# Optimization experiments

Measured on AMD Instinct MI355X. Metric: run time of the kernel, lower is better.

Reference implementation:

```python
import jax, jax.numpy as jnp
import numpy as np

N = 100000      # nodes
E = 1600000     # edges (avg degree 16)
D_IN, D_H, D_OUT = 128, 64, 40


def setup_inputs() -> dict:
    key = jax.random.key(0)
    ks = jax.random.split(key, 9)
    x = jax.random.normal(ks[0], (N, D_IN), dtype=jnp.float32)
    edge_index = jax.random.randint(ks[1], (2, E), 0, N)
    affected_mask = jax.random.randint(ks[2], (N,), 0, 2).astype(bool)
    # GCNConv weights stored as [in, out]
    Wc1 = jax.random.normal(ks[3], (D_IN, D_H), jnp.float32) / np.sqrt(D_IN)
    bc1 = jax.random.normal(ks[4], (D_H,), jnp.float32) * 0.01
    Wc2 = jax.random.normal(ks[5], (D_H, D_OUT), jnp.float32) / np.sqrt(D_H)
    bc2 = jax.random.normal(ks[6], (D_OUT,), jnp.float32) * 0.01
    # deletion operators initialized to identity (per nn.init.eye_/zeros_)
    Wd1 = jnp.eye(D_H, dtype=jnp.float32)
    bd1 = jnp.zeros((D_H,), jnp.float32)
    Wd2 = jnp.eye(D_OUT, dtype=jnp.float32)
    bd2 = jnp.zeros((D_OUT,), jnp.float32)
    return {"x": x, "edge_index": edge_index, "affected_mask": affected_mask,
            "Wc1": Wc1, "bc1": bc1, "Wc2": Wc2, "bc2": bc2,
            "Wd1": Wd1, "bd1": bd1, "Wd2": Wd2, "bd2": bd2}


def _gcn_norm(edge_index, n):
    # add self loops, compute symmetric normalization coefficients
    loop = jnp.arange(n)
    src = jnp.concatenate([edge_index[0], loop])
    dst = jnp.concatenate([edge_index[1], loop])
    deg = jax.ops.segment_sum(jnp.ones_like(src, jnp.float32), dst, num_segments=n)
    dinv = jnp.where(deg > 0, jax.lax.rsqrt(deg), 0.0)
    norm = dinv[src] * dinv[dst]  # [E+N]
    return src, dst, norm


def _gcn_conv(h, src, dst, norm, W, b, n):
    hw = h @ W                              # [N, d_out]
    msg = hw[src] * norm[:, None]           # gather + scale  [E+N, d_out]
    return jax.ops.segment_sum(msg, dst, num_segments=n) + b


def reference(x, edge_index, affected_mask, Wc1, bc1, Wc2, bc2, Wd1, bd1, Wd2, bd2):
    n = x.shape[0]
    src, dst, norm = _gcn_norm(edge_index, n)
    h = jax.nn.relu(_gcn_conv(x, src, dst, norm, Wc1, bc1, n))
    # eval-mode dropout == identity
    # deletion op 1: masked gather -> linear -> scatter == masked select
    m1 = affected_mask[:, None]
    h_del = jnp.where(m1, h @ Wd1.T + bd1, h)
    out = _gcn_conv(h_del, src, dst, norm, Wc2, bc2, n)
    out_del = jnp.where(m1, out @ Wd2.T + bd2, out)
    return out_del
```

## Files before the change

### kernel.cpp

```cpp
#include <hip/hip_runtime.h>

#define D_IN  128
#define D_H   64
#define D_OUT 40

__device__ __forceinline__ float bf_lo(unsigned u){ return __uint_as_float(u << 16); }
__device__ __forceinline__ float bf_hi(unsigned u){ return __uint_as_float(u & 0xFFFF0000u); }
__device__ __forceinline__ unsigned bf_pack(float a, float b){
  unsigned ua = __float_as_uint(a), ub = __float_as_uint(b);
  unsigned lo = (ua + 0x7FFFu + ((ua >> 16) & 1u)) >> 16;
  unsigned hi = (ub + 0x7FFFu + ((ub >> 16) & 1u)) & 0xFFFF0000u;
  return hi | lo;
}


__launch_bounds__(256)
static __global__ void k_degpos(const int* __restrict__ dst, int* __restrict__ deg,
                                int* __restrict__ pos, int E){
  int base = (blockIdx.x*256 + threadIdx.x) * 4;
  if (base + 4 <= E){
    int4 d = *(const int4*)(dst + base);
    int4 p;
    p.x = atomicAdd(&deg[d.x], 1);
    p.y = atomicAdd(&deg[d.y], 1);
    p.z = atomicAdd(&deg[d.z], 1);
    p.w = atomicAdd(&deg[d.w], 1);
    *(int4*)(pos + base) = p;
  } else {
    for (int i = base; i < E; i++) pos[i] = atomicAdd(&deg[dst[i]], 1);
  }
}

static __global__ void k_scan1(const int* __restrict__ deg, int* __restrict__ incl,
                               int* __restrict__ bsums, int n){
  __shared__ int s[1024];
  int t = threadIdx.x; int g = blockIdx.x*1024 + t;
  int v = (g < n) ? deg[g] : 0;
  s[t] = v; __syncthreads();
  for (int off = 1; off < 1024; off <<= 1){
    int u = (t >= off) ? s[t-off] : 0; __syncthreads();
    s[t] += u; __syncthreads();
  }
  if (g < n) incl[g] = s[t];
  if (t == 1023) bsums[blockIdx.x] = s[1023];
}

static __global__ void k_scan2(int* bsums, int nb){
  __shared__ int s[128];
  int t = threadIdx.x;
  int v = (t < nb) ? bsums[t] : 0;
  s[t] = v; __syncthreads();
  for (int off = 1; off < 128; off <<= 1){
    int u = (t >= off) ? s[t-off] : 0; __syncthreads();
    s[t] += u; __syncthreads();
  }
  if (t < nb) bsums[t] = s[t] - v;
}

static __global__ void k_scan3(const int* __restrict__ deg, int* __restrict__ rs,
                               const int* __restrict__ bsums,
                               float* __restrict__ dinv, int n){
  int t = threadIdx.x; int g = blockIdx.x*1024 + t;
  if (g < n){
    int excl = rs[g] - deg[g] + bsums[blockIdx.x];
    rs[g] = excl;
    dinv[g] = rsqrtf((float)(deg[g] + 1));
  }
}

__launch_bounds__(256)
static __global__ void k_scatter(const int* __restrict__ src, const int* __restrict__ dst,
                                 const int* __restrict__ pos, const int* __restrict__ rs,
                                 int* __restrict__ col, int E){
  int base = (blockIdx.x*256 + threadIdx.x) * 4;
  if (base + 4 <= E){
    int4 d = *(const int4*)(dst + base);
    int4 s = *(const int4*)(src + base);
    int4 p = *(const int4*)(pos + base);
    col[rs[d.x] + p.x] = s.x;
    col[rs[d.y] + p.y] = s.y;
    col[rs[d.z] + p.z] = s.z;
    col[rs[d.w] + p.w] = s.w;
  } else {
    for (int i = base; i < E; i++) col[rs[dst[i]] + pos[i]] = src[i];
  }
}


static __global__ void k_pre(const float* __restrict__ Wd1, const float* __restrict__ bd1,
                             const float* __restrict__ Wc2, float* __restrict__ M,
                             float* __restrict__ bvec){
  int t = threadIdx.x;
  for (int i = t; i < D_H*D_OUT; i += 256){
    int q = i / D_OUT, j = i % D_OUT;
    float s = 0.f;
    for (int k = 0; k < D_H; k++) s += Wd1[k*D_H + q] * Wc2[k*D_OUT + j];
    M[i] = s;
  }
  if (t < D_OUT){
    float s = 0.f;
    for (int k = 0; k < D_H; k++) s += bd1[k] * Wc2[k*D_OUT + t];
    bvec[t] = s;
  }
}


__launch_bounds__(256)
static __global__ void k_gemm1(const float* __restrict__ x, const float* __restrict__ Wc1,
                               const float* __restrict__ dinv,
                               unsigned short* __restrict__ hws1b, int n){
  __shared__ float Wl[D_IN*D_H];
  __shared__ float xs[32][D_IN+1];
  int t = threadIdx.x;
  int base = blockIdx.x*32;
  for (int i = t; i < D_IN*D_H; i += 256) Wl[i] = Wc1[i];
  for (int i = t; i < 32*D_IN; i += 256){
    int r = i >> 7, c = i & 127;
    int node = base + r;
    xs[r][c] = (node < n) ? x[(size_t)node*D_IN + c] : 0.f;
  }
  __syncthreads();
  int nl = t >> 3, j0 = (t & 7)*8;
  int node = base + nl;
  if (node >= n) return;
  float acc[8] = {0,0,0,0,0,0,0,0};
  #pragma unroll 4
  for (int k = 0; k < D_IN; k++){
    float xv = xs[nl][k];
    #pragma unroll
    for (int jj = 0; jj < 8; jj++) acc[jj] += xv * Wl[k*D_H + j0 + jj];
  }
  float dv = dinv[node];
  uint4 o;
  o.x = bf_pack(acc[0]*dv, acc[1]*dv);
  o.y = bf_pack(acc[2]*dv, acc[3]*dv);
  o.z = bf_pack(acc[4]*dv, acc[5]*dv);
  o.w = bf_pack(acc[6]*dv, acc[7]*dv);
  *(uint4*)(hws1b + (size_t)node*D_H + j0) = o;
}


__launch_bounds__(256)
static __global__ void k_agg1(const unsigned short* __restrict__ hws1b, const int* __restrict__ rs,
                              const int* __restrict__ deg, const int* __restrict__ col,
                              const float* __restrict__ dinv, const float* __restrict__ bc1,
                              float* __restrict__ h, int n){
  int t = threadIdx.x;
  int wave = t >> 6, lane = t & 63;
  int node = blockIdx.x*4 + wave;
  if (node >= n) return;
  int grp = lane >> 4, fl = lane & 15;
  const uint2* g2 = (const uint2*)hws1b;
  float a0=0.f, a1=0.f, a2=0.f, a3=0.f;
  if (grp == 0){
    uint2 v = g2[(size_t)node*16 + fl];
    a0 += bf_lo(v.x); a1 += bf_hi(v.x); a2 += bf_lo(v.y); a3 += bf_hi(v.y);
  }
  int s0 = rs[node], cnt = deg[node];
  #pragma unroll 4
  for (int e0 = 0; e0 < cnt; e0 += 4){
    int sl = e0 + grp;
    if (sl < cnt){
      int s = col[s0 + sl];
      uint2 v = g2[(size_t)s*16 + fl];
      a0 += bf_lo(v.x); a1 += bf_hi(v.x); a2 += bf_lo(v.y); a3 += bf_hi(v.y);
    }
  }
  a0 += __shfl_xor(a0, 16, 64); a1 += __shfl_xor(a1, 16, 64);
  a2 += __shfl_xor(a2, 16, 64); a3 += __shfl_xor(a3, 16, 64);
  a0 += __shfl_xor(a0, 32, 64); a1 += __shfl_xor(a1, 32, 64);
  a2 += __shfl_xor(a2, 32, 64); a3 += __shfl_xor(a3, 32, 64);
  if (grp == 0){
    float dv = dinv[node];
    float4 b = ((const float4*)bc1)[fl];
    float4 o;
    o.x = fmaxf(a0*dv + b.x, 0.f);
    o.y = fmaxf(a1*dv + b.y, 0.f);
    o.z = fmaxf(a2*dv + b.z, 0.f);
    o.w = fmaxf(a3*dv + b.w, 0.f);
    ((float4*)h)[(size_t)node*16 + fl] = o;
  }
}


__launch_bounds__(128)
static __global__ void k_gemm2(const float* __restrict__ h, const unsigned char* __restrict__ mask,
                               const float* __restrict__ Mmat, const float* __restrict__ bvec,
                               const float* __restrict__ Wc2, const float* __restrict__ dinv,
                               unsigned short* __restrict__ hws2b, int n){
  __shared__ float Ms[D_H*D_OUT];
  __shared__ float Ws[D_H*D_OUT];
  __shared__ float bv[D_OUT];
  __shared__ float hs[128*(D_H+1)];
  int t = threadIdx.x;
  int base = blockIdx.x*128;
  for (int i = t; i < D_H*D_OUT; i += 128){ Ms[i] = Mmat[i]; Ws[i] = Wc2[i]; }
  if (t < D_OUT) bv[t] = bvec[t];
  for (int i = t; i < 128*D_H; i += 128){
    int r = i >> 6, c = i & 63;
    int node = base + r;
    hs[r*(D_H+1) + c] = (node < n) ? h[(size_t)node*D_H + c] : 0.f;
  }
  __syncthreads();
  int node = base + t;
  if (node >= n) return;
  bool m = mask[node] != 0;
  const float* Wp = m ? Ms : Ws;
  float acc[D_OUT];
  #pragma unroll
  for (int j = 0; j < D_OUT; j++) acc[j] = m ? bv[j] : 0.f;
  const float* hrow = &hs[t*(D_H+1)];
  for (int q = 0; q < D_H; q++){
    float hv = hrow[q];
    #pragma unroll
    for (int j = 0; j < D_OUT; j++) acc[j] += hv * Wp[q*D_OUT + j];
  }
  float dv = dinv[node];
  unsigned short* op = hws2b + (size_t)node*D_OUT;
  #pragma unroll
  for (int k = 0; k < 5; k++){
    uint4 o;
    o.x = bf_pack(acc[k*8+0]*dv, acc[k*8+1]*dv);
    o.y = bf_pack(acc[k*8+2]*dv, acc[k*8+3]*dv);
    o.z = bf_pack(acc[k*8+4]*dv, acc[k*8+5]*dv);
    o.w = bf_pack(acc[k*8+6]*dv, acc[k*8+7]*dv);
    *(uint4*)(op + k*8) = o;
  }
}


__launch_bounds__(256)
static __global__ void k_agg2(const unsigned short* __restrict__ hws2b, const int* __restrict__ rs,
                              const int* __restrict__ deg, const int* __restrict__ col,
                              const float* __restrict__ dinv, const float* __restrict__ bc2,
                              const unsigned char* __restrict__ mask,
                              const float* __restrict__ Wd2, const float* __restrict__ bd2,
                              float* __restrict__ out, int n){
  __shared__ float4 wds4[D_OUT*11];
  __shared__ float  bds[D_OUT];
  __shared__ float4 os4[4][11];
  int t = threadIdx.x;
  for (int i = t; i < D_OUT*10; i += 256){
    int j = i / 10, q = i % 10;
    const float* wr = Wd2 + j*D_OUT + q*4;
    wds4[j*11 + q] = make_float4(wr[0], wr[1], wr[2], wr[3]);
  }
  if (t < D_OUT) bds[t] = bd2[t];
  __syncthreads();
  int wave = t >> 6, lane = t & 63;
  int node = blockIdx.x*4 + wave;
  if (node >= n) return;
  int grp = lane >> 4, fl = lane & 15;
  bool fa = fl < 10;
  const uint2* g2 = (const uint2*)hws2b;
  float a0=0.f, a1=0.f, a2=0.f, a3=0.f;
  if (grp == 0 && fa){
    uint2 v = g2[(size_t)node*10 + fl];
    a0 += bf_lo(v.x); a1 += bf_hi(v.x); a2 += bf_lo(v.y); a3 += bf_hi(v.y);
  }
  int s0 = rs[node], cnt = deg[node];
  #pragma unroll 4
  for (int e0 = 0; e0 < cnt; e0 += 4){
    int sl = e0 + grp;
    if (sl < cnt && fa){
      int s = col[s0 + sl];
      uint2 v = g2[(size_t)s*10 + fl];
      a0 += bf_lo(v.x); a1 += bf_hi(v.x); a2 += bf_lo(v.y); a3 += bf_hi(v.y);
    }
  }
  a0 += __shfl_xor(a0, 16, 64); a1 += __shfl_xor(a1, 16, 64);
  a2 += __shfl_xor(a2, 16, 64); a3 += __shfl_xor(a3, 16, 64);
  a0 += __shfl_xor(a0, 32, 64); a1 += __shfl_xor(a1, 32, 64);
  a2 += __shfl_xor(a2, 32, 64); a3 += __shfl_xor(a3, 32, 64);
  float dv = dinv[node];
  float4 res = make_float4(0.f, 0.f, 0.f, 0.f);
  if (fa){
    float4 b = ((const float4*)bc2)[fl];
    res.x = a0*dv + b.x;
    res.y = a1*dv + b.y;
    res.z = a2*dv + b.z;
    res.w = a3*dv + b.w;
  }
  if (mask[node] != 0){
    if (grp == 0 && fa) os4[wave][fl] = res;
    int J = grp*10 + fl;
    float r = 0.f;
    if (fa) r = bds[J];
    #pragma unroll
    for (int q = 0; q < 10; q++){
      float4 hv = os4[wave][q];
      if (fa){
        float4 wv = wds4[J*11 + q];
        r += hv.x*wv.x + hv.y*wv.y + hv.z*wv.z + hv.w*wv.w;
      }
    }
    if (fa) out[(size_t)node*D_OUT + J] = r;
  } else if (grp == 0 && fa){
    ((float4*)out)[(size_t)node*10 + fl] = res;
  }
}


extern "C" void kernel_launch(void* const* d_in, const int* in_sizes, int n_in,
                              void* d_out, int out_size, void* d_ws, size_t ws_size,
                              hipStream_t stream){
  const float* x    = (const float*)d_in[0];
  const int*   ei   = (const int*)d_in[1];
  const unsigned char* mask = (const unsigned char*)d_in[2];
  const float* Wc1  = (const float*)d_in[3];
  const float* bc1  = (const float*)d_in[4];
  const float* Wc2  = (const float*)d_in[5];
  const float* bc2  = (const float*)d_in[6];
  const float* Wd1  = (const float*)d_in[7];
  const float* bd1  = (const float*)d_in[8];
  const float* Wd2  = (const float*)d_in[9];
  const float* bd2  = (const float*)d_in[10];

  int N = in_sizes[0] / D_IN;
  int E = in_sizes[1] / 2;
  const int* src = ei;
  const int* dst = ei + E;
  float* out = (float*)d_out;

  char* w = (char*)d_ws; size_t off = 0;
  auto A = [&](size_t bytes)->void*{
    void* p = w + off;
    off += (bytes + 255) & ~(size_t)255;
    return p;
  };
  int*   deg    = (int*)  A((size_t)N*4);
  int*   rs     = (int*)  A((size_t)N*4);
  int*   bsums  = (int*)  A(256*4);
  float* dinv   = (float*)A((size_t)N*4);
  float* Mmat   = (float*)A((size_t)D_H*D_OUT*4);
  float* bvec   = (float*)A((size_t)D_OUT*4);
  int*   col    = (int*)  A((size_t)E*4);
  unsigned short* hws1b = (unsigned short*)A((size_t)N*D_H*2);
  float* h      = (float*)A((size_t)N*D_H*4);
  unsigned short* hws2b = hws1b;
  int*   pos    = (int*)hws1b;

  int NB  = (N + 1023) / 1024;
  int EB4 = (E + 1023) / 1024;

  hipMemsetAsync(deg, 0, (size_t)N*4, stream);
  hipLaunchKernelGGL(k_degpos, dim3(EB4), dim3(256), 0, stream, dst, deg, pos, E);
  hipLaunchKernelGGL(k_scan1, dim3(NB), dim3(1024), 0, stream, deg, rs, bsums, N);
  hipLaunchKernelGGL(k_scan2, dim3(1), dim3(128), 0, stream, bsums, NB);
  hipLaunchKernelGGL(k_scan3, dim3(NB), dim3(1024), 0, stream, deg, rs, bsums, dinv, N);
  hipLaunchKernelGGL(k_scatter, dim3(EB4), dim3(256), 0, stream, src, dst, pos, rs, col, E);
  hipLaunchKernelGGL(k_pre,   dim3(1), dim3(256), 0, stream, Wd1, bd1, Wc2, Mmat, bvec);
  hipLaunchKernelGGL(k_gemm1, dim3((N+31)/32), dim3(256), 0, stream, x, Wc1, dinv, hws1b, N);
  hipLaunchKernelGGL(k_agg1,  dim3((N+3)/4), dim3(256), 0, stream, hws1b, rs, deg, col, dinv, bc1, h, N);
  hipLaunchKernelGGL(k_gemm2, dim3((N+127)/128), dim3(128), 0, stream, h, mask, Mmat, bvec, Wc2, dinv, hws2b, N);
  hipLaunchKernelGGL(k_agg2,  dim3((N+3)/4), dim3(256), 0, stream, hws2b, rs, deg, col, dinv, bc2, mask, Wd2, bd2, out, N);
}
```

Before: 498.1 us.

## Split gathered features into column slabs and aggregate each slab separately

Bf16 message buffers are stored as four column slabs (16 or 12 features per node) instead of full rows. Each aggregation block now handles one slab for a group of nodes, and block indices are interleaved so the slabs are processed close together in time. The aim is for each slab's gather working set to stay resident in cache, which would cut random-access traffic to HBM. The price is re-reading the CSR indices four times, splitting the second aggregation from the deletion-op post-processing (an extra kernel plus an fp32 temp round trip), and padding layer-2 slabs from 40 to 48 features.

Result: slower. 640.4 us (+28.6%).

```diff
diff --git a/kernel.cpp b/kernel.cpp
--- a/kernel.cpp
+++ b/kernel.cpp
@@ -108,7 +108,7 @@
 __launch_bounds__(256)
 static __global__ void k_gemm1(const float* __restrict__ x, const float* __restrict__ Wc1,
                                const float* __restrict__ dinv,
-                               unsigned short* __restrict__ hws1b, int n){
+                               unsigned short* __restrict__ hq1, int n, int Q1){
   __shared__ float Wl[D_IN*D_H];
   __shared__ float xs[32][D_IN+1];
   int t = threadIdx.x;
@@ -136,49 +136,57 @@
   o.y = bf_pack(acc[2]*dv, acc[3]*dv);
   o.z = bf_pack(acc[4]*dv, acc[5]*dv);
   o.w = bf_pack(acc[6]*dv, acc[7]*dv);
-  *(uint4*)(hws1b + (size_t)node*D_H + j0) = o;
-}
-
-
-__launch_bounds__(256)
-static __global__ void k_agg1(const unsigned short* __restrict__ hws1b, const int* __restrict__ rs,
+  int q = j0 >> 4;
+  *(uint4*)(hq1 + (size_t)q*Q1 + (size_t)node*16 + (j0 & 15)) = o;
+}
+
+
+__launch_bounds__(256)
+static __global__ void k_agg1(const unsigned short* __restrict__ hq1, const int* __restrict__ rs,
                               const int* __restrict__ deg, const int* __restrict__ col,
                               const float* __restrict__ dinv, const float* __restrict__ bc1,
-                              float* __restrict__ h, int n){
+                              float* __restrict__ h, int n, int Q1){
+  int b = blockIdx.x;
+  int q = (b & 7) >> 1;
+  int j = ((b >> 3) << 1) | (b & 1);
   int t = threadIdx.x;
   int wave = t >> 6, lane = t & 63;
-  int node = blockIdx.x*4 + wave;
-  if (node >= n) return;
-  int grp = lane >> 4, fl = lane & 15;
-  const uint2* g2 = (const uint2*)hws1b;
+  int node = j*4 + wave;
+  if (node >= n) return;
+  int grp = lane >> 2, fl = lane & 3;
+  const uint2* g2 = (const uint2*)(hq1 + (size_t)q*Q1);
   float a0=0.f, a1=0.f, a2=0.f, a3=0.f;
   if (grp == 0){
-    uint2 v = g2[(size_t)node*16 + fl];
+    uint2 v = g2[(size_t)node*4 + fl];
     a0 += bf_lo(v.x); a1 += bf_hi(v.x); a2 += bf_lo(v.y); a3 += bf_hi(v.y);
   }
   int s0 = rs[node], cnt = deg[node];
-  #pragma unroll 4
-  for (int e0 = 0; e0 < cnt; e0 += 4){
+  #pragma unroll 2
+  for (int e0 = 0; e0 < cnt; e0 += 16){
     int sl = e0 + grp;
     if (sl < cnt){
       int s = col[s0 + sl];
-      uint2 v = g2[(size_t)s*16 + fl];
+      uint2 v = g2[(size_t)s*4 + fl];
       a0 += bf_lo(v.x); a1 += bf_hi(v.x); a2 += bf_lo(v.y); a3 += bf_hi(v.y);
     }
   }
+  a0 += __shfl_xor(a0,  4, 64); a1 += __shfl_xor(a1,  4, 64);
+  a2 += __shfl_xor(a2,  4, 64); a3 += __shfl_xor(a3,  4, 64);
+  a0 += __shfl_xor(a0,  8, 64); a1 += __shfl_xor(a1,  8, 64);
+  a2 += __shfl_xor(a2,  8, 64); a3 += __shfl_xor(a3,  8, 64);
   a0 += __shfl_xor(a0, 16, 64); a1 += __shfl_xor(a1, 16, 64);
   a2 += __shfl_xor(a2, 16, 64); a3 += __shfl_xor(a3, 16, 64);
   a0 += __shfl_xor(a0, 32, 64); a1 += __shfl_xor(a1, 32, 64);
   a2 += __shfl_xor(a2, 32, 64); a3 += __shfl_xor(a3, 32, 64);
   if (grp == 0){
     float dv = dinv[node];
-    float4 b = ((const float4*)bc1)[fl];
+    float4 bb = *(const float4*)(bc1 + q*16 + fl*4);
     float4 o;
-    o.x = fmaxf(a0*dv + b.x, 0.f);
-    o.y = fmaxf(a1*dv + b.y, 0.f);
-    o.z = fmaxf(a2*dv + b.z, 0.f);
-    o.w = fmaxf(a3*dv + b.w, 0.f);
-    ((float4*)h)[(size_t)node*16 + fl] = o;
+    o.x = fmaxf(a0*dv + bb.x, 0.f);
+    o.y = fmaxf(a1*dv + bb.y, 0.f);
+    o.z = fmaxf(a2*dv + bb.z, 0.f);
+    o.w = fmaxf(a3*dv + bb.w, 0.f);
+    *(float4*)(h + (size_t)node*D_H + q*16 + fl*4) = o;
   }
 }
 
@@ -187,7 +195,7 @@
 static __global__ void k_gemm2(const float* __restrict__ h, const unsigned char* __restrict__ mask,
                                const float* __restrict__ Mmat, const float* __restrict__ bvec,
                                const float* __restrict__ Wc2, const float* __restrict__ dinv,
-                               unsigned short* __restrict__ hws2b, int n){
+                               unsigned short* __restrict__ hq2, int n, int Q2){
   __shared__ float Ms[D_H*D_OUT];
   __shared__ float Ws[D_H*D_OUT];
   __shared__ float bv[D_OUT];
@@ -210,30 +218,83 @@
   #pragma unroll
   for (int j = 0; j < D_OUT; j++) acc[j] = m ? bv[j] : 0.f;
   const float* hrow = &hs[t*(D_H+1)];
-  for (int q = 0; q < D_H; q++){
-    float hv = hrow[q];
+  for (int qq = 0; qq < D_H; qq++){
+    float hv = hrow[qq];
     #pragma unroll
-    for (int j = 0; j < D_OUT; j++) acc[j] += hv * Wp[q*D_OUT + j];
+    for (int j = 0; j < D_OUT; j++) acc[j] += hv * Wp[qq*D_OUT + j];
   }
   float dv = dinv[node];
-  unsigned short* op = hws2b + (size_t)node*D_OUT;
   #pragma unroll
-  for (int k = 0; k < 5; k++){
-    uint4 o;
-    o.x = bf_pack(acc[k*8+0]*dv, acc[k*8+1]*dv);
-    o.y = bf_pack(acc[k*8+2]*dv, acc[k*8+3]*dv);
-    o.z = bf_pack(acc[k*8+4]*dv, acc[k*8+5]*dv);
-    o.w = bf_pack(acc[k*8+6]*dv, acc[k*8+7]*dv);
-    *(uint4*)(op + k*8) = o;
-  }
-}
-
-
-__launch_bounds__(256)
-static __global__ void k_agg2(const unsigned short* __restrict__ hws2b, const int* __restrict__ rs,
+  for (int q = 0; q < 4; q++){
+    unsigned short* op = hq2 + (size_t)q*Q2 + (size_t)node*12;
+    #pragma unroll
+    for (int k = 0; k < 3; k++){
+      int j = q*12 + k*4;
+      float f0 = (j+0 < D_OUT) ? acc[j+0]*dv : 0.f;
+      float f1 = (j+1 < D_OUT) ? acc[j+1]*dv : 0.f;
+      float f2 = (j+2 < D_OUT) ? acc[j+2]*dv : 0.f;
+      float f3 = (j+3 < D_OUT) ? acc[j+3]*dv : 0.f;
+      uint2 o; o.x = bf_pack(f0, f1); o.y = bf_pack(f2, f3);
+      *(uint2*)(op + k*4) = o;
+    }
+  }
+}
+
+
+__launch_bounds__(256)
+static __global__ void k_agg2(const unsigned short* __restrict__ hq2, const int* __restrict__ rs,
                               const int* __restrict__ deg, const int* __restrict__ col,
                               const float* __restrict__ dinv, const float* __restrict__ bc2,
-                              const unsigned char* __restrict__ mask,
+                              float* __restrict__ tmp, int n, int Q2){
+  int b = blockIdx.x;
+  int q = (b & 7) >> 1;
+  int j = ((b >> 3) << 1) | (b & 1);
+  int t = threadIdx.x;
+  int wave = t >> 6, lane = t & 63;
+  int node = j*4 + wave;
+  if (node >= n) return;
+  int grp = lane >> 2, fl = lane & 3;
+  bool fa = fl < 3;
+  const uint2* g2 = (const uint2*)(hq2 + (size_t)q*Q2);
+  float a0=0.f, a1=0.f, a2=0.f, a3=0.f;
+  if (grp == 0 && fa){
+    uint2 v = g2[(size_t)node*3 + fl];
+    a0 += bf_lo(v.x); a1 += bf_hi(v.x); a2 += bf_lo(v.y); a3 += bf_hi(v.y);
+  }
+  int s0 = rs[node], cnt = deg[node];
+  #pragma unroll 2
+  for (int e0 = 0; e0 < cnt; e0 += 16){
+    int sl = e0 + grp;
+    if (sl < cnt && fa){
+      int s = col[s0 + sl];
+      uint2 v = g2[(size_t)s*3 + fl];
+      a0 += bf_lo(v.x); a1 += bf_hi(v.x); a2 += bf_lo(v.y); a3 += bf_hi(v.y);
+    }
+  }
+  a0 += __shfl_xor(a0,  4, 64); a1 += __shfl_xor(a1,  4, 64);
+  a2 += __shfl_xor(a2,  4, 64); a3 += __shfl_xor(a3,  4, 64);
+  a0 += __shfl_xor(a0,  8, 64); a1 += __shfl_xor(a1,  8, 64);
+  a2 += __shfl_xor(a2,  8, 64); a3 += __shfl_xor(a3,  8, 64);
+  a0 += __shfl_xor(a0, 16, 64); a1 += __shfl_xor(a1, 16, 64);
+  a2 += __shfl_xor(a2, 16, 64); a3 += __shfl_xor(a3, 16, 64);
+  a0 += __shfl_xor(a0, 32, 64); a1 += __shfl_xor(a1, 32, 64);
+  a2 += __shfl_xor(a2, 32, 64); a3 += __shfl_xor(a3, 32, 64);
+  int j0 = q*12 + fl*4;
+  if (grp == 0 && fa && j0 < D_OUT){
+    float dv = dinv[node];
+    float4 bb = *(const float4*)(bc2 + j0);
+    float4 o;
+    o.x = a0*dv + bb.x;
+    o.y = a1*dv + bb.y;
+    o.z = a2*dv + bb.z;
+    o.w = a3*dv + bb.w;
+    *(float4*)(tmp + (size_t)node*D_OUT + j0) = o;
+  }
+}
+
+
+__launch_bounds__(256)
+static __global__ void k_post(const float* __restrict__ tmp, const unsigned char* __restrict__ mask,
                               const float* __restrict__ Wd2, const float* __restrict__ bd2,
                               float* __restrict__ out, int n){
   __shared__ float4 wds4[D_OUT*11];
@@ -241,62 +302,30 @@
   __shared__ float4 os4[4][11];
   int t = threadIdx.x;
   for (int i = t; i < D_OUT*10; i += 256){
-    int j = i / 10, q = i % 10;
-    const float* wr = Wd2 + j*D_OUT + q*4;
-    wds4[j*11 + q] = make_float4(wr[0], wr[1], wr[2], wr[3]);
+    int jj = i / 10, qq = i % 10;
+    const float* wr = Wd2 + jj*D_OUT + qq*4;
+    wds4[jj*11 + qq] = make_float4(wr[0], wr[1], wr[2], wr[3]);
   }
   if (t < D_OUT) bds[t] = bd2[t];
   __syncthreads();
   int wave = t >> 6, lane = t & 63;
   int node = blockIdx.x*4 + wave;
   if (node >= n) return;
-  int grp = lane >> 4, fl = lane & 15;
-  bool fa = fl < 10;
-  const uint2* g2 = (const uint2*)hws2b;
-  float a0=0.f, a1=0.f, a2=0.f, a3=0.f;
-  if (grp == 0 && fa){
-    uint2 v = g2[(size_t)node*10 + fl];
-    a0 += bf_lo(v.x); a1 += bf_hi(v.x); a2 += bf_lo(v.y); a3 += bf_hi(v.y);
-  }
-  int s0 = rs[node], cnt = deg[node];
-  #pragma unroll 4
-  for (int e0 = 0; e0 < cnt; e0 += 4){
-    int sl = e0 + grp;
-    if (sl < cnt && fa){
-      int s = col[s0 + sl];
-      uint2 v = g2[(size_t)s*10 + fl];
-      a0 += bf_lo(v.x); a1 += bf_hi(v.x); a2 += bf_lo(v.y); a3 += bf_hi(v.y);
-    }
-  }
-  a0 += __shfl_xor(a0, 16, 64); a1 += __shfl_xor(a1, 16, 64);
-  a2 += __shfl_xor(a2, 16, 64); a3 += __shfl_xor(a3, 16, 64);
-  a0 += __shfl_xor(a0, 32, 64); a1 += __shfl_xor(a1, 32, 64);
-  a2 += __shfl_xor(a2, 32, 64); a3 += __shfl_xor(a3, 32, 64);
-  float dv = dinv[node];
-  float4 res = make_float4(0.f, 0.f, 0.f, 0.f);
-  if (fa){
-    float4 b = ((const float4*)bc2)[fl];
-    res.x = a0*dv + b.x;
-    res.y = a1*dv + b.y;
-    res.z = a2*dv + b.z;
-    res.w = a3*dv + b.w;
-  }
+  const float4* trow = (const float4*)(tmp + (size_t)node*D_OUT);
   if (mask[node] != 0){
-    if (grp == 0 && fa) os4[wave][fl] = res;
-    int J = grp*10 + fl;
-    float r = 0.f;
-    if (fa) r = bds[J];
+    if (lane < 10) os4[wave][lane] = trow[lane];
+    float r = (lane < D_OUT) ? bds[lane] : 0.f;
     #pragma unroll
-    for (int q = 0; q < 10; q++){
-      float4 hv = os4[wave][q];
-      if (fa){
-        float4 wv = wds4[J*11 + q];
+    for (int qq = 0; qq < 10; qq++){
+      float4 hv = os4[wave][qq];
+      if (lane < D_OUT){
+        float4 wv = wds4[lane*11 + qq];
         r += hv.x*wv.x + hv.y*wv.y + hv.z*wv.z + hv.w*wv.w;
       }
     }
-    if (fa) out[(size_t)node*D_OUT + J] = r;
-  } else if (grp == 0 && fa){
-    ((float4*)out)[(size_t)node*10 + fl] = res;
+    if (lane < D_OUT) out[(size_t)node*D_OUT + lane] = r;
+  } else {
+    if (lane < 10) ((float4*)(out + (size_t)node*D_OUT))[lane] = trow[lane];
   }
 }
 
@@ -335,13 +364,19 @@
   float* Mmat   = (float*)A((size_t)D_H*D_OUT*4);
   float* bvec   = (float*)A((size_t)D_OUT*4);
   int*   col    = (int*)  A((size_t)E*4);
-  unsigned short* hws1b = (unsigned short*)A((size_t)N*D_H*2);
+  unsigned short* hq1 = (unsigned short*)A((size_t)N*64*2);
   float* h      = (float*)A((size_t)N*D_H*4);
-  unsigned short* hws2b = hws1b;
-  int*   pos    = (int*)hws1b;
+  unsigned short* hq2 = hq1;
+  int*   pos    = (int*)hq1;
+  float* tmp    = h;
+
+  int Q1 = N*16;
+  int Q2 = N*12;
 
   int NB  = (N + 1023) / 1024;
   int EB4 = (E + 1023) / 1024;
+  int nb4 = (N + 3) / 4;
+  int GA  = ((nb4 + 1) / 2) * 8;
 
   hipMemsetAsync(deg, 0, (size_t)N*4, stream);
   hipLaunchKernelGGL(k_degpos, dim3(EB4), dim3(256), 0, stream, dst, deg, pos, E);
@@ -350,8 +385,9 @@
   hipLaunchKernelGGL(k_scan3, dim3(NB), dim3(1024), 0, stream, deg, rs, bsums, dinv, N);
   hipLaunchKernelGGL(k_scatter, dim3(EB4), dim3(256), 0, stream, src, dst, pos, rs, col, E);
   hipLaunchKernelGGL(k_pre,   dim3(1), dim3(256), 0, stream, Wd1, bd1, Wc2, Mmat, bvec);
-  hipLaunchKernelGGL(k_gemm1, dim3((N+31)/32), dim3(256), 0, stream, x, Wc1, dinv, hws1b, N);
-  hipLaunchKernelGGL(k_agg1,  dim3((N+3)/4), dim3(256), 0, stream, hws1b, rs, deg, col, dinv, bc1, h, N);
-  hipLaunchKernelGGL(k_gemm2, dim3((N+127)/128), dim3(128), 0, stream, h, mask, Mmat, bvec, Wc2, dinv, hws2b, N);
-  hipLaunchKernelGGL(k_agg2,  dim3((N+3)/4), dim3(256), 0, stream, hws2b, rs, deg, col, dinv, bc2, mask, Wd2, bd2, out, N);
-}
+  hipLaunchKernelGGL(k_gemm1, dim3((N+31)/32), dim3(256), 0, stream, x, Wc1, dinv, hq1, N, Q1);
+  hipLaunchKernelGGL(k_agg1,  dim3(GA), dim3(256), 0, stream, hq1, rs, deg, col, dinv, bc1, h, N, Q1);
+  hipLaunchKernelGGL(k_gemm2, dim3((N+127)/128), dim3(128), 0, stream, h, mask, Mmat, bvec, Wc2, dinv, hq2, N, Q2);
+  hipLaunchKernelGGL(k_agg2,  dim3(GA), dim3(256), 0, stream, hq2, rs, deg, col, dinv, bc2, tmp, N, Q2);
+  hipLaunchKernelGGL(k_post,  dim3(nb4), dim3(256), 0, stream, tmp, mask, Wd2, bd2, out, N);
+}
```
